# Optimization experiments

Hardware: AMD Instinct MI355X
Metric: run time of the kernel (lower is better)

## Reference

```python
import jax, jax.numpy as jnp
import numpy as np

D_MODEL = 2048
N_HEADS = 16
D_K = D_MODEL // N_HEADS
MAX_SEQ_LEN = 2048


def _rotary_tables(dim, max_seq_len):
    angular_freq = (1.0 / 10000.0) ** jnp.linspace(0.0, 1.0, dim // 2, dtype=jnp.float32)
    t = jnp.arange(max_seq_len, dtype=jnp.float32)
    theta = jnp.einsum('i,j->ij', t, angular_freq)  # [S, dk/2]
    return jnp.cos(theta), jnp.sin(theta)


def _apply_rotary(x, cos, sin):
    # x: [B, H, S, dk]; cos/sin: [S, dk/2]
    seq_len = x.shape[-2]
    c = cos[:seq_len][None, None]
    s = sin[:seq_len][None, None]
    x1, x2 = jnp.split(x, 2, axis=-1)
    y1 = x1 * c - x2 * s
    y2 = x1 * s + x2 * c
    return jnp.concatenate([y1, y2], axis=-1).astype(x.dtype)


def setup_inputs() -> dict:
    key = jax.random.key(0)
    k_x, k_qkv, k_o = jax.random.split(key, 3)
    B, S = 2, 2048
    x = jax.random.normal(k_x, (B, S, D_MODEL), dtype=jnp.float32)
    scale = 1.0 / np.sqrt(D_MODEL)
    w_qkv = jax.random.normal(k_qkv, (3 * D_MODEL, D_MODEL), dtype=jnp.float32) * scale
    w_o = jax.random.normal(k_o, (D_MODEL, D_MODEL), dtype=jnp.float32) * scale
    return {"x": x, "w_qkv": w_qkv, "w_o": w_o}


def reference(x, w_qkv, w_o):
    B, S, _ = x.shape
    cos, sin = _rotary_tables(D_K, MAX_SEQ_LEN)
    qkv = jnp.einsum('bsd,ed->bse', x, w_qkv)  # [B, S, 3*d_model]
    qkv = qkv.reshape(B, S, 3, N_HEADS, D_K).transpose(2, 0, 3, 1, 4)  # [3,B,H,S,dk]
    Q, K, V = qkv[0], qkv[1], qkv[2]
    Q = _apply_rotary(Q, cos, sin)
    K = _apply_rotary(K, cos, sin)
    scale = 1.0 / np.sqrt(D_K)
    scores = jnp.einsum('bhqd,bhkd->bhqk', Q, K) * scale
    causal = jnp.tril(jnp.ones((S, S), dtype=bool))
    scores = jnp.where(causal[None, None], scores, jnp.finfo(scores.dtype).min)
    attn = jax.nn.softmax(scores, axis=-1)
    out = jnp.einsum('bhqk,bhkd->bhqd', attn, V)  # [B,H,S,dk]
    out = out.transpose(0, 2, 1, 3).reshape(B, S, D_MODEL)
    return jnp.einsum('bsd,ed->bse', out, w_o)
```

## Files before the change

kernel.cpp:

```cpp
#include <hip/hip_runtime.h>
#include <hip/hip_bf16.h>


typedef __bf16 bf16;
typedef __bf16 bf16x4 __attribute__((ext_vector_type(4)));
typedef __bf16 bf16x8 __attribute__((ext_vector_type(8)));
typedef float f32x4 __attribute__((ext_vector_type(4)));
typedef float f32x16 __attribute__((ext_vector_type(16)));
typedef int i32x4 __attribute__((ext_vector_type(4)));

#define DEV __device__ __forceinline__

DEV void gll16(const void* g, void* lds_base_wave_uniform) {
  __builtin_amdgcn_global_load_lds((const __attribute__((address_space(1))) void*)g,
                                   (__attribute__((address_space(3))) void*)lds_base_wave_uniform,
                                   16, 0, 0);
}

DEV f32x4 mfma16(bf16x8 a, bf16x8 b, f32x4 c) {
  return __builtin_amdgcn_mfma_f32_16x16x32_bf16(a, b, c, 0, 0, 0);
}
DEV f32x16 mfma32(bf16x8 a, bf16x8 b, f32x16 c) {
  return __builtin_amdgcn_mfma_f32_32x32x16_bf16(a, b, c, 0, 0, 0);
}

DEV int cvtpk(float lo, float hi) {
  int r;
  asm("v_cvt_pk_bf16_f32 %0, %1, %2" : "=v"(r) : "v"(lo), "v"(hi));
  return r;
}

__global__ __launch_bounds__(256) void prep_all(const float* __restrict__ x,
                                                const float* __restrict__ wqkv,
                                                const float* __restrict__ wo,
                                                bf16* __restrict__ xb,
                                                bf16* __restrict__ wqkvb,
                                                bf16* __restrict__ wob,
                                                float* __restrict__ ctab,
                                                float* __restrict__ stab) {
  const int b = blockIdx.x;
  if (b < 12288) {
    const float* in;
    bf16* out;
    int bb = b;
    if (b < 4096) {
      in = x; out = xb;
    } else if (b < 10240) {
      in = wqkv; out = wqkvb; bb -= 4096;
    } else {
      in = wo; out = wob; bb -= 10240;
    }
    const int i = (bb * 256 + threadIdx.x) << 3;
    float4 a = *(const float4*)(in + i);
    float4 c = *(const float4*)(in + i + 4);
    bf16x8 o;
    o[0] = (bf16)a.x; o[1] = (bf16)a.y; o[2] = (bf16)a.z; o[3] = (bf16)a.w;
    o[4] = (bf16)c.x; o[5] = (bf16)c.y; o[6] = (bf16)c.z; o[7] = (bf16)c.w;
    *(bf16x8*)(out + i) = o;
  } else {
    const int id = (b - 12288) * 256 + threadIdx.x;
    const int s = id >> 6, j = id & 63;
    float freq = powf(10000.0f, -(float)j / 63.0f);
    float th = (float)s * freq;
    ctab[id] = cosf(th);
    stab[id] = sinf(th);
  }
}

__global__ __launch_bounds__(512, 2) void gemm384(const bf16* __restrict__ A,
                                                  const bf16* __restrict__ Bt,
                                                  bf16* __restrict__ q_out,
                                                  bf16* __restrict__ k_out,
                                                  bf16* __restrict__ v_out,
                                                  const float* __restrict__ ctab,
                                                  const float* __restrict__ stab) {
  constexpr int K = 2048, NKT = 64;
  constexpr int BUFB = 40960;
  __shared__ char lds[3 * BUFB];
  const int id = blockIdx.x;
  const int swz = (id & 7) * 32 + (id >> 3);
  const int bx = swz & 15, by = swz >> 4;
  const int m0 = by << 8;
  const int n0 = bx * 384;
  const int tid = threadIdx.x, w = tid >> 6, l = tid & 63;
  const int wm = w >> 2, wn = w & 3;
  const int lsl = (l & 7) ^ ((l >> 3) & 7);
  const int srow = ((l >> 3) << 1) + (lsl >> 2);
  const int scol = (lsl & 3) << 3;

  auto STAGE = [&](int t, char* base) {
    const int k0 = t << 5;
#pragma unroll
    for (int c = 0; c < 2; ++c) {
      const int row = (c << 7) + (w << 4) + srow;
      gll16(A + (size_t)(m0 + row) * K + k0 + scol, base + (c << 13) + (w << 10));
    }
#pragma unroll
    for (int c = 0; c < 3; ++c) {
      const int row = (c << 7) + (w << 4) + srow;
      gll16(Bt + (size_t)(n0 + row) * K + k0 + scol, base + 16384 + (c << 13) + (w << 10));
    }
  };

  f32x4 acc[8][6] = {};

  STAGE(0, (char*)lds);
  STAGE(1, (char*)lds + BUFB);
  asm volatile("s_waitcnt vmcnt(5)" ::: "memory");
  __builtin_amdgcn_s_barrier();

#pragma unroll 1
  for (int t = 0, bi = 0, bj = 2; t < NKT; ++t) {
    char* rbase = (char*)lds + bi * BUFB;
    bf16x8 bfr[6];
#pragma unroll
    for (int j = 0; j < 6; ++j) {
      const int row = ((j >> 1) << 7) + ((j & 1) << 6) + (wn << 4) + (l & 15);
      const int sr = row >> 1;
      bfr[j] = *(const bf16x8*)(rbase + 16384 + sr * 128 +
                                (((((row & 1) << 2) | (l >> 4)) ^ (sr & 7)) << 4));
    }
    bf16x8 af[4];
#pragma unroll
    for (int i = 0; i < 4; ++i) {
      const int row = (wm << 7) + (i << 4) + (l & 15);
      const int sr = row >> 1;
      af[i] = *(const bf16x8*)(rbase + sr * 128 +
                               (((((row & 1) << 2) | (l >> 4)) ^ (sr & 7)) << 4));
    }
    if (t + 2 < NKT) STAGE(t + 2, (char*)lds + bj * BUFB);
    asm volatile("s_waitcnt lgkmcnt(0)" ::: "memory");
    __builtin_amdgcn_sched_barrier(0);
    __builtin_amdgcn_s_setprio(1);
#pragma unroll
    for (int i = 0; i < 4; ++i)
#pragma unroll
      for (int j = 0; j < 6; ++j)
        acc[i][j] = mfma16(af[i], bfr[j], acc[i][j]);
    __builtin_amdgcn_s_setprio(0);
#pragma unroll
    for (int i = 0; i < 4; ++i) {
      const int row = (wm << 7) + 64 + (i << 4) + (l & 15);
      const int sr = row >> 1;
      af[i] = *(const bf16x8*)(rbase + sr * 128 +
                               (((((row & 1) << 2) | (l >> 4)) ^ (sr & 7)) << 4));
    }
    asm volatile("s_waitcnt lgkmcnt(0)" ::: "memory");
    __builtin_amdgcn_sched_barrier(0);
    __builtin_amdgcn_s_setprio(1);
#pragma unroll
    for (int i = 0; i < 4; ++i)
#pragma unroll
      for (int j = 0; j < 6; ++j)
        acc[4 + i][j] = mfma16(af[i], bfr[j], acc[4 + i][j]);
    __builtin_amdgcn_s_setprio(0);
    if (t + 2 < NKT) {
      asm volatile("s_waitcnt vmcnt(5)" ::: "memory");
    } else if (t + 2 == NKT) {
      asm volatile("s_waitcnt vmcnt(0)" ::: "memory");
    }
    __builtin_amdgcn_sched_barrier(0);
    __builtin_amdgcn_s_barrier();
    bi = (bi == 2) ? 0 : bi + 1;
    bj = (bj == 2) ? 0 : bj + 1;
  }

  const int d2 = (wn << 4) + (l & 15);
#pragma unroll
  for (int i = 0; i < 8; ++i) {
    const int mbase = m0 + (wm << 7) + (i << 4) + ((l >> 4) << 2);
    const int b_ = mbase >> 11, sbase = mbase & 2047;
    float cc[4], ss[4];
    if (((n0 + 256) >> 11) == 1 || (n0 >> 11) == 1) {
#pragma unroll
      for (int r = 0; r < 4; ++r) {
        cc[r] = ctab[((sbase + r) << 6) + d2];
        ss[r] = stab[((sbase + r) << 6) + d2];
      }
    }
#pragma unroll
    for (int p = 0; p < 3; ++p) {
      const int nb = n0 + (p << 7);
      const int which = nb >> 11;
      const int h = (nb >> 7) & 15;
      if (which == 0) {
        const size_t base = (((size_t)((b_ << 4) | h)) * 2048 + sbase) * 128;
#pragma unroll
        for (int r = 0; r < 4; ++r) {
          q_out[base + ((size_t)r << 7) + d2]      = (bf16)acc[i][2 * p][r];
          q_out[base + ((size_t)r << 7) + d2 + 64] = (bf16)acc[i][2 * p + 1][r];
        }
      } else if (which == 1) {
        const size_t base = (((size_t)((b_ << 4) | h)) * 2048 + sbase) * 128;
#pragma unroll
        for (int r = 0; r < 4; ++r) {
          const float x1 = acc[i][2 * p][r], x2 = acc[i][2 * p + 1][r];
          k_out[base + ((size_t)r << 7) + d2]      = (bf16)(x1 * cc[r] - x2 * ss[r]);
          k_out[base + ((size_t)r << 7) + d2 + 64] = (bf16)(x1 * ss[r] + x2 * cc[r]);
        }
      } else {
        bf16x4 v1, v2;
#pragma unroll
        for (int r = 0; r < 4; ++r) {
          v1[r] = (bf16)acc[i][2 * p][r];
          v2[r] = (bf16)acc[i][2 * p + 1][r];
        }
        const size_t hb = ((size_t)((b_ << 4) | h) << 18);
        *(bf16x4*)(v_out + hb + ((size_t)d2 << 11) + sbase) = v1;
        *(bf16x4*)(v_out + hb + ((size_t)(d2 + 64) << 11) + sbase) = v2;
      }
    }
  }
}

template <int NTN>
__global__ __launch_bounds__(256, 2) void gemm_o(const bf16* __restrict__ A,
                                                 const bf16* __restrict__ Bt,
                                                 float* __restrict__ f_out) {
  constexpr int K = 2048, NKT = 64;
  constexpr int BUFB = 16384;
  __shared__ char lds[3 * BUFB];
  const int nwg = 32 * NTN;
  const int id = blockIdx.x;
  const int swz = (id & 7) * (nwg >> 3) + (id >> 3);
  const int bx = swz % NTN, by = swz / NTN;
  const int m0 = by << 7, n0 = bx << 7;
  const int tid = threadIdx.x, w = tid >> 6, l = tid & 63;
  const int wm = w >> 1, wn = w & 1;
  const int lsl = (l & 7) ^ ((l >> 3) & 7);
  const int srow = ((l >> 3) << 1) + (lsl >> 2);
  const int scol = (lsl & 3) << 3;

  auto STAGE = [&](int t, char* base) {
    const int k0 = t << 5;
#pragma unroll
    for (int c = 0; c < 2; ++c) {
      const int row = (c << 6) + (w << 4) + srow;
      gll16(A + (size_t)(m0 + row) * K + k0 + scol, base + (c << 12) + (w << 10));
      gll16(Bt + (size_t)(n0 + row) * K + k0 + scol, base + 8192 + (c << 12) + (w << 10));
    }
  };

  f32x4 acc[4][4] = {};

  STAGE(0, (char*)lds);
  STAGE(1, (char*)lds + BUFB);
  asm volatile("s_waitcnt vmcnt(4)" ::: "memory");
  __builtin_amdgcn_s_barrier();

#pragma unroll 1
  for (int t = 0, bi = 0, bj = 2; t < NKT; ++t) {
    char* rbase = (char*)lds + bi * BUFB;
    bf16x8 af[4], bfr[4];
#pragma unroll
    for (int i = 0; i < 4; ++i) {
      const int row = (wm << 6) + (i << 4) + (l & 15);
      const int sr = row >> 1;
      af[i] = *(const bf16x8*)(rbase + sr * 128 +
                               (((((row & 1) << 2) | (l >> 4)) ^ (sr & 7)) << 4));
    }
#pragma unroll
    for (int j = 0; j < 4; ++j) {
      const int row = (wn << 6) + (j << 4) + (l & 15);
      const int sr = row >> 1;
      bfr[j] = *(const bf16x8*)(rbase + 8192 + sr * 128 +
                                (((((row & 1) << 2) | (l >> 4)) ^ (sr & 7)) << 4));
    }
    if (t + 2 < NKT) STAGE(t + 2, (char*)lds + bj * BUFB);
    asm volatile("s_waitcnt lgkmcnt(0)" ::: "memory");
    __builtin_amdgcn_sched_barrier(0);
    __builtin_amdgcn_s_setprio(1);
#pragma unroll
    for (int i = 0; i < 4; ++i)
#pragma unroll
      for (int j = 0; j < 4; ++j)
        acc[i][j] = mfma16(af[i], bfr[j], acc[i][j]);
    __builtin_amdgcn_s_setprio(0);
    if (t + 2 < NKT) {
      asm volatile("s_waitcnt vmcnt(4)" ::: "memory");
    } else if (t + 2 == NKT) {
      asm volatile("s_waitcnt vmcnt(0)" ::: "memory");
    }
    __builtin_amdgcn_sched_barrier(0);
    __builtin_amdgcn_s_barrier();
    bi = (bi == 2) ? 0 : bi + 1;
    bj = (bj == 2) ? 0 : bj + 1;
  }

#pragma unroll
  for (int i = 0; i < 4; ++i)
#pragma unroll
    for (int j = 0; j < 4; ++j)
#pragma unroll
      for (int r = 0; r < 4; ++r) {
        const int m = m0 + (wm << 6) + (i << 4) + ((l >> 4) << 2) + r;
        const int n = n0 + (wn << 6) + (j << 4) + (l & 15);
        f_out[(size_t)m * 2048 + n] = acc[i][j][r];
      }
}

__global__ __launch_bounds__(256, 2) void attn_kernel(const bf16* __restrict__ Qb,
                                                      const bf16* __restrict__ Kb,
                                                      const bf16* __restrict__ Vt,
                                                      bf16* __restrict__ Ao,
                                                      const float* __restrict__ ctab,
                                                      const float* __restrict__ stab) {
  constexpr int S = 2048;
  __shared__ bf16 Ks[2][64 * 128];
  __shared__ bf16 Vs[2][128 * 64];
  const int id = blockIdx.x;
  const int swz = (id & 7) * 64 + (id >> 3);
  const int bh = swz >> 4;
  int qt = swz & 15;
  if ((swz >> 5) & 1) qt = 15 - qt;
  const int q0 = qt << 7;
  const int tid = threadIdx.x, w = tid >> 6, l = tid & 63;
  const int hi = l >> 5;
  const bf16* Qp = Qb + ((size_t)bh << 18);
  const bf16* Kp = Kb + ((size_t)bh << 18);
  const bf16* Vp = Vt + ((size_t)bh << 18);

  auto STAGE_KV = [&](int kv0, int bufi) {
    char* Kbase = (char*)Ks + (bufi << 14);
    char* Vbase = (char*)Vs + (bufi << 14);
#pragma unroll
    for (int i = 0; i < 4; ++i) {
      const int rk = (w << 4) + (i << 2) + (l >> 4);
      gll16(Kp + ((size_t)(kv0 + rk) << 7) + (((l & 15) ^ (rk & 7)) << 3),
            Kbase + (w << 12) + (i << 10));
      const int rv = (w << 5) + (i << 3) + (l >> 3);
      gll16(Vp + (size_t)rv * S + kv0 + (((l & 7) ^ (rv & 7)) << 3),
            Vbase + (w << 12) + (i << 10));
    }
  };

  STAGE_KV(0, 0);

  const int sq = q0 + (w << 5) + (l & 31);
  bf16x8 qf[8];
#pragma unroll
  for (int kt = 0; kt < 8; ++kt)
    qf[kt] = *(const bf16x8*)(Qp + ((size_t)sq << 7) + (kt << 4) + (hi << 3));
  {
    const float QS = 0.08838834764831845f * 1.4426950408889634f;
#pragma unroll
    for (int kt = 0; kt < 4; ++kt) {
      const int d2 = (kt << 4) + (hi << 3);
      const float* cp = ctab + (sq << 6) + d2;
      const float* sp = stab + (sq << 6) + d2;
      float4 c0 = *(const float4*)cp, c1 = *(const float4*)(cp + 4);
      float4 s0 = *(const float4*)sp, s1 = *(const float4*)(sp + 4);
      const float cA[8] = {c0.x, c0.y, c0.z, c0.w, c1.x, c1.y, c1.z, c1.w};
      const float sA[8] = {s0.x, s0.y, s0.z, s0.w, s1.x, s1.y, s1.z, s1.w};
      const bf16x8 lo = qf[kt], up = qf[kt + 4];
#pragma unroll
      for (int j2 = 0; j2 < 8; ++j2) {
        const float a = (float)lo[j2], b2 = (float)up[j2];
        qf[kt][j2]     = (bf16)((a * cA[j2] - b2 * sA[j2]) * QS);
        qf[kt + 4][j2] = (bf16)((a * sA[j2] + b2 * cA[j2]) * QS);
      }
    }
  }

  f32x16 o[4] = {};
  float mrun = -3e38f, lrun = 0.f;

  const int qminw = q0 + (w << 5);
  const int qmaxw = qminw + 31;
  const int kv_end = q0 + 128;

  __syncthreads();

  int bufi = 0;
#pragma unroll 1
  for (int kv0 = 0; kv0 < kv_end; kv0 += 64, bufi ^= 1) {
    if (kv0 + 64 < kv_end) STAGE_KV(kv0 + 64, bufi ^ 1);
    if (kv0 <= qmaxw) {
      const char* Kbase = (const char*)Ks + (bufi << 14);
      const char* Vbase = (const char*)Vs + (bufi << 14);
      f32x16 sc0 = {}, sc1 = {};
      __builtin_amdgcn_s_setprio(1);
#pragma unroll
      for (int kt = 0; kt < 8; ++kt) {
        const int rk0 = l & 31;
        const int coff = ((kt << 5) + (hi << 4));
        bf16x8 k0 = *(const bf16x8*)(Kbase + (rk0 << 8) + (coff ^ ((rk0 & 7) << 4)));
        bf16x8 k1 = *(const bf16x8*)(Kbase + ((rk0 + 32) << 8) + (coff ^ ((rk0 & 7) << 4)));
        sc0 = mfma32(k0, qf[kt], sc0);
        sc1 = mfma32(k1, qf[kt], sc1);
      }
      __builtin_amdgcn_s_setprio(0);
      if (kv0 + 63 > qminw) {
        const int qg = qminw + (l & 31);
#pragma unroll
        for (int r = 0; r < 16; ++r) {
          const int kvr = kv0 + (r & 3) + ((r >> 2) << 3) + (hi << 2);
          if (kvr > qg) sc0[r] = -3e38f;
          if (kvr + 32 > qg) sc1[r] = -3e38f;
        }
      }
      float mx = -3e38f;
#pragma unroll
      for (int r = 0; r < 16; ++r) mx = fmaxf(mx, fmaxf(sc0[r], sc1[r]));
      mx = fmaxf(mx, __shfl_xor(mx, 32));
      const float mnew = fmaxf(mrun, mx);
      if (!__all(mx <= mrun)) {
        const float alpha = exp2f(mrun - mnew);
        lrun *= alpha;
#pragma unroll
        for (int dt = 0; dt < 4; ++dt) o[dt] *= alpha;
      }
      mrun = mnew;
      float ps = 0.f;
#pragma unroll
      for (int r = 0; r < 16; ++r) {
        sc0[r] = exp2f(sc0[r] - mnew); ps += sc0[r];
        sc1[r] = exp2f(sc1[r] - mnew); ps += sc1[r];
      }
      ps += __shfl_xor(ps, 32);
      lrun += ps;
#pragma unroll
      for (int ks = 0; ks < 4; ++ks) {
        const f32x16& s = (ks & 2) ? sc1 : sc0;
        const int rb = (ks & 1) << 3;
        int pa_ = cvtpk(s[rb + 0], s[rb + 1]);
        int pb_ = cvtpk(s[rb + 2], s[rb + 3]);
        int pc_ = cvtpk(s[rb + 4], s[rb + 5]);
        int pd_ = cvtpk(s[rb + 6], s[rb + 7]);
        int sa = __shfl_xor(pa_, 32), sb = __shfl_xor(pb_, 32);
        int sc_ = __shfl_xor(pc_, 32), sd = __shfl_xor(pd_, 32);
        i32x4 pi;
        pi[0] = hi ? sc_ : pa_;
        pi[1] = hi ? sd : pb_;
        pi[2] = hi ? pc_ : sa;
        pi[3] = hi ? pd_ : sb;
        const bf16x8 pf = __builtin_bit_cast(bf16x8, pi);
        __builtin_amdgcn_s_setprio(1);
#pragma unroll
        for (int dt = 0; dt < 4; ++dt) {
          const int rd = (dt << 5) + (l & 31);
          const bf16x8 vf = *(const bf16x8*)(Vbase + (rd << 7) +
                                             (((ks << 5) + (hi << 4)) ^ ((rd & 7) << 4)));
          o[dt] = mfma32(vf, pf, o[dt]);
        }
        __builtin_amdgcn_s_setprio(0);
      }
    }
    __syncthreads();
  }
  const float rinv = 1.0f / lrun;
  const int b = bh >> 4, h = bh & 15;
  bf16* Arow = Ao + (((size_t)(b * S + sq)) << 11) + (h << 7);
#pragma unroll
  for (int dt = 0; dt < 4; ++dt)
#pragma unroll
    for (int g = 0; g < 4; ++g) {
      bf16x4 ov;
#pragma unroll
      for (int r = 0; r < 4; ++r) ov[r] = (bf16)(o[dt][(g << 2) + r] * rinv);
      *(bf16x4*)(Arow + (dt << 5) + (g << 3) + (hi << 2)) = ov;
    }
}

extern "C" void kernel_launch(void* const* d_in, const int* in_sizes, int n_in,
                              void* d_out, int out_size, void* d_ws, size_t ws_size,
                              hipStream_t stream) {
  const float* x = (const float*)d_in[0];
  const float* w_qkv = (const float*)d_in[1];
  const float* w_o = (const float*)d_in[2];
  float* out = (float*)d_out;
  char* ws = (char*)d_ws;

  bf16* xb    = (bf16*)(ws);
  bf16* wqkvb = (bf16*)(ws + (16ull << 20));
  bf16* wob   = (bf16*)(ws + (40ull << 20));
  bf16* Qb    = (bf16*)(ws + (48ull << 20));
  bf16* Kb    = (bf16*)(ws + (64ull << 20));
  bf16* Vt    = (bf16*)(ws + (80ull << 20));
  bf16* Ao    = (bf16*)(ws + (96ull << 20));
  float* ctab = (float*)(ws + (112ull << 20));
  float* stab = (float*)(ws + (113ull << 20));

  prep_all<<<12800, 256, 0, stream>>>(x, w_qkv, w_o, xb, wqkvb, wob, ctab, stab);
  gemm384<<<256, 512, 0, stream>>>(xb, wqkvb, Qb, Kb, Vt, ctab, stab);
  attn_kernel<<<512, 256, 0, stream>>>(Qb, Kb, Vt, Ao, ctab, stab);
  gemm_o<16><<<512, 256, 0, stream>>>(Ao, wob, out);
}
```

Baseline: 244.9 us.

## Pair complementary causal query tiles per attention block for balanced work

```diff
diff --git a/kernel.cpp b/kernel.cpp
--- a/kernel.cpp
+++ b/kernel.cpp
@@ -309,11 +309,11 @@
   __shared__ bf16 Ks[2][64 * 128];
   __shared__ bf16 Vs[2][128 * 64];
   const int id = blockIdx.x;
-  const int swz = (id & 7) * 64 + (id >> 3);
-  const int bh = swz >> 4;
-  int qt = swz & 15;
-  if ((swz >> 5) & 1) qt = 15 - qt;
-  const int q0 = qt << 7;
+  const int swz = (id & 7) * 32 + (id >> 3);
+  const int bh = swz >> 3;
+  const int pp = swz & 7;
+  const int ntA = (pp + 1) << 1;
+  const int NT = 34;
   const int tid = threadIdx.x, w = tid >> 6, l = tid & 63;
   const int hi = l >> 5;
   const bf16* Qp = Qb + ((size_t)bh << 18);
@@ -334,14 +334,12 @@
     }
   };
 
-  STAGE_KV(0, 0);
-
-  const int sq = q0 + (w << 5) + (l & 31);
   bf16x8 qf[8];
-#pragma unroll
-  for (int kt = 0; kt < 8; ++kt)
-    qf[kt] = *(const bf16x8*)(Qp + ((size_t)sq << 7) + (kt << 4) + (hi << 3));
-  {
+  auto LOAD_Q = [&](int q0_) {
+    const int sq = q0_ + (w << 5) + (l & 31);
+#pragma unroll
+    for (int kt = 0; kt < 8; ++kt)
+      qf[kt] = *(const bf16x8*)(Qp + ((size_t)sq << 7) + (kt << 4) + (hi << 3));
     const float QS = 0.08838834764831845f * 1.4426950408889634f;
 #pragma unroll
     for (int kt = 0; kt < 4; ++kt) {
@@ -360,22 +358,42 @@
         qf[kt + 4][j2] = (bf16)((a * sA[j2] + b2 * cA[j2]) * QS);
       }
     }
-  }
+  };
 
   f32x16 o[4] = {};
   float mrun = -3e38f, lrun = 0.f;
-
-  const int qminw = q0 + (w << 5);
-  const int qmaxw = qminw + 31;
-  const int kv_end = q0 + 128;
-
+  int q0 = pp << 7;
+
+  auto EPILOGUE = [&](int q0_) {
+    const float rinv = 1.0f / lrun;
+    const int b = bh >> 4, h = bh & 15;
+    const int sq = q0_ + (w << 5) + (l & 31);
+    bf16* Arow = Ao + (((size_t)(b * S + sq)) << 11) + (h << 7);
+#pragma unroll
+    for (int dt = 0; dt < 4; ++dt)
+#pragma unroll
+      for (int g = 0; g < 4; ++g) {
+        bf16x4 ov;
+#pragma unroll
+        for (int r = 0; r < 4; ++r) ov[r] = (bf16)(o[dt][(g << 2) + r] * rinv);
+        *(bf16x4*)(Arow + (dt << 5) + (g << 3) + (hi << 2)) = ov;
+      }
+  };
+
+  STAGE_KV(0, 0);
+  LOAD_Q(q0);
   __syncthreads();
 
   int bufi = 0;
 #pragma unroll 1
-  for (int kv0 = 0; kv0 < kv_end; kv0 += 64, bufi ^= 1) {
-    if (kv0 + 64 < kv_end) STAGE_KV(kv0 + 64, bufi ^ 1);
-    if (kv0 <= qmaxw) {
+  for (int ti = 0; ti < NT; ++ti, bufi ^= 1) {
+    const int kv0 = ((ti < ntA) ? ti : ti - ntA) << 6;
+    if (ti + 1 < NT) {
+      const int kv0n = ((ti + 1 < ntA) ? ti + 1 : ti + 1 - ntA) << 6;
+      STAGE_KV(kv0n, bufi ^ 1);
+    }
+    const int qminw = q0 + (w << 5);
+    if (kv0 <= qminw + 31) {
       const char* Kbase = (const char*)Ks + (bufi << 14);
       const char* Vbase = (const char*)Vs + (bufi << 14);
       f32x16 sc0 = {}, sc1 = {};
@@ -399,9 +417,14 @@
           if (kvr + 32 > qg) sc1[r] = -3e38f;
         }
       }
-      float mx = -3e38f;
-#pragma unroll
-      for (int r = 0; r < 16; ++r) mx = fmaxf(mx, fmaxf(sc0[r], sc1[r]));
+      f32x16 mm;
+#pragma unroll
+      for (int r = 0; r < 16; ++r) mm[r] = fmaxf(sc0[r], sc1[r]);
+#pragma unroll
+      for (int off = 8; off; off >>= 1)
+#pragma unroll
+        for (int r = 0; r < off; ++r) mm[r] = fmaxf(mm[r], mm[r + off]);
+      float mx = mm[0];
       mx = fmaxf(mx, __shfl_xor(mx, 32));
       const float mnew = fmaxf(mrun, mx);
       if (!__all(mx <= mrun)) {
@@ -411,12 +434,14 @@
         for (int dt = 0; dt < 4; ++dt) o[dt] *= alpha;
       }
       mrun = mnew;
-      float ps = 0.f;
-#pragma unroll
-      for (int r = 0; r < 16; ++r) {
-        sc0[r] = exp2f(sc0[r] - mnew); ps += sc0[r];
-        sc1[r] = exp2f(sc1[r] - mnew); ps += sc1[r];
-      }
+      float p0 = 0.f, p1 = 0.f, p2 = 0.f, p3 = 0.f;
+#pragma unroll
+      for (int r = 0; r < 16; r += 2) {
+        sc0[r] = exp2f(sc0[r] - mnew); sc0[r + 1] = exp2f(sc0[r + 1] - mnew);
+        sc1[r] = exp2f(sc1[r] - mnew); sc1[r + 1] = exp2f(sc1[r + 1] - mnew);
+        p0 += sc0[r]; p1 += sc0[r + 1]; p2 += sc1[r]; p3 += sc1[r + 1];
+      }
+      float ps = (p0 + p1) + (p2 + p3);
       ps += __shfl_xor(ps, 32);
       lrun += ps;
 #pragma unroll
@@ -446,20 +471,19 @@
         __builtin_amdgcn_s_setprio(0);
       }
     }
+    if (ti == ntA - 1) {
+      EPILOGUE(q0);
+      q0 = (15 - pp) << 7;
+#pragma unroll
+      for (int dt = 0; dt < 4; ++dt)
+#pragma unroll
+        for (int r = 0; r < 16; ++r) o[dt][r] = 0.f;
+      mrun = -3e38f; lrun = 0.f;
+      LOAD_Q(q0);
+    }
     __syncthreads();
   }
-  const float rinv = 1.0f / lrun;
-  const int b = bh >> 4, h = bh & 15;
-  bf16* Arow = Ao + (((size_t)(b * S + sq)) << 11) + (h << 7);
-#pragma unroll
-  for (int dt = 0; dt < 4; ++dt)
-#pragma unroll
-    for (int g = 0; g < 4; ++g) {
-      bf16x4 ov;
-#pragma unroll
-      for (int r = 0; r < 4; ++r) ov[r] = (bf16)(o[dt][(g << 2) + r] * rinv);
-      *(bf16x4*)(Arow + (dt << 5) + (g << 3) + (hi << 2)) = ov;
-    }
+  EPILOGUE(q0);
 }
 
 extern "C" void kernel_launch(void* const* d_in, const int* in_sizes, int n_in,
@@ -483,6 +507,6 @@
 
   prep_all<<<12800, 256, 0, stream>>>(x, w_qkv, w_o, xb, wqkvb, wob, ctab, stab);
   gemm384<<<256, 512, 0, stream>>>(xb, wqkvb, Qb, Kb, Vt, ctab, stab);
-  attn_kernel<<<512, 256, 0, stream>>>(Qb, Kb, Vt, Ao, ctab, stab);
+  attn_kernel<<<256, 256, 0, stream>>>(Qb, Kb, Vt, Ao, ctab, stab);
   gemm_o<16><<<512, 256, 0, stream>>>(Ao, wob, out);
 }
```

Result: no change. 244.1 us (-0.3%).
